# Performance work log

Measured on AMD Instinct MI355X. Metric: run time of the kernel, lower is better.

The kernel has to match this reference:

```python
import jax, jax.numpy as jnp
import numpy as np

B, T, C = 4, 2048, 768
N_HEAD = 12
HEAD_DIM = C // N_HEAD


def setup_inputs() -> dict:
    key = jax.random.key(0)
    k1, k2, k3 = jax.random.split(key, 3)
    x = jax.random.normal(k1, (B, T, C), dtype=jnp.float32)
    w_attn = jax.random.normal(k2, (C, 3 * C), dtype=jnp.float32) * (1.0 / np.sqrt(C))
    b_attn = jnp.zeros((3 * C,), dtype=jnp.float32)
    w_proj = jax.random.normal(k3, (C, C), dtype=jnp.float32) * (1.0 / np.sqrt(C))
    b_proj = jnp.zeros((C,), dtype=jnp.float32)
    return {"x": x, "w_attn": w_attn, "b_attn": b_attn, "w_proj": w_proj, "b_proj": b_proj}


def reference(x, w_attn, b_attn, w_proj, b_proj):
    # x: [B, T, C]
    Bs, Ts, Cs = x.shape
    qkv = x @ w_attn + b_attn                         # [B, T, 3C]
    q, k, v = jnp.split(qkv, 3, axis=-1)
    # -> [B, H, T, Dh]
    q = q.reshape(Bs, Ts, N_HEAD, HEAD_DIM).swapaxes(1, 2)
    k = k.reshape(Bs, Ts, N_HEAD, HEAD_DIM).swapaxes(1, 2)
    v = v.reshape(Bs, Ts, N_HEAD, HEAD_DIM).swapaxes(1, 2)
    scale = 1.0 / jnp.sqrt(jnp.asarray(HEAD_DIM, dtype=x.dtype))
    att = jnp.einsum('bhqd,bhkd->bhqk', q, k) * scale  # [B, H, T, T]
    causal = jnp.tril(jnp.ones((Ts, Ts), dtype=bool))[None, None]
    att = jnp.where(causal, att, jnp.asarray(-jnp.inf, dtype=att.dtype))
    att = jax.nn.softmax(att, axis=-1)
    y = jnp.einsum('bhqk,bhkd->bhqd', att, v)          # [B, H, T, Dh]
    y = y.swapaxes(1, 2).reshape(Bs, Ts, Cs)
    y = y @ w_proj + b_proj
    return y
```

## Files before the change

### kernel.cpp

```cpp
#include <hip/hip_runtime.h>
#include <cstdint>
#include <cstddef>

typedef __bf16 bf16x8 __attribute__((ext_vector_type(8)));
typedef float  f32x4  __attribute__((ext_vector_type(4)));
typedef unsigned short us;

#define DEV static __device__ __forceinline__

DEV us f2bf(float f) {
    unsigned int u = __builtin_bit_cast(unsigned int, f);
    u += 0x7FFFu + ((u >> 16) & 1u);
    return (us)(u >> 16);
}
DEV unsigned int pack2bf(float a, float b) {
    unsigned int ua = __builtin_bit_cast(unsigned int, a) + 0x8000u;
    unsigned int ub = __builtin_bit_cast(unsigned int, b) + 0x8000u;
    return (ua >> 16) | (ub & 0xFFFF0000u);
}

DEV void gll16(const void* g, void* l) {
    __builtin_amdgcn_global_load_lds(
        (const __attribute__((address_space(1))) unsigned int*)g,
        (__attribute__((address_space(3))) unsigned int*)l, 16, 0, 0);
}

DEV bf16x8 ld_frag(const us* p) {
    return __builtin_bit_cast(bf16x8, *reinterpret_cast<const uint4*>(p));
}

#define BB 4
#define TT 2048
#define CC 768
#define NH 12
#define DH 64
#define MM (BB*TT)
#define QSCALE 0.1803368801111144f

__global__ __launch_bounds__(256)
void cast_k(const float* __restrict__ x, us* __restrict__ xb, int n4)
{
    int i = blockIdx.x * 256 + threadIdx.x;
    int stride = gridDim.x * 256;
    for (; i < n4; i += stride) {
        float4 f = reinterpret_cast<const float4*>(x)[i];
        ushort4 o;
        o.x = f2bf(f.x); o.y = f2bf(f.y); o.z = f2bf(f.z); o.w = f2bf(f.w);
        reinterpret_cast<ushort4*>(xb)[i] = o;
    }
}

__global__ __launch_bounds__(256)
void transpose_k(const float* __restrict__ src,
                 us* __restrict__ dst, int R, int Cc)
{
    __shared__ float tile[32][33];
    int c0 = blockIdx.x * 32, r0 = blockIdx.y * 32;
    int tx = threadIdx.x, ty = threadIdx.y;
#pragma unroll
    for (int i = 0; i < 4; ++i)
        tile[ty + i*8][tx] = src[(size_t)(r0 + ty + i*8) * Cc + c0 + tx];
    __syncthreads();
#pragma unroll
    for (int i = 0; i < 4; ++i)
        dst[(size_t)(c0 + ty + i*8) * R + r0 + tx] = f2bf(tile[tx][ty + i*8]);
}


#define BM 128
#define BN 128
#define BK 32

template<int MODE>
__global__ __launch_bounds__(256)
void gemm_bt(const us* __restrict__ A,
             const us* __restrict__ Bt,
             const float* __restrict__ bias,
             float* __restrict__ Cout,
             us* __restrict__ Qo, us* __restrict__ Ko, us* __restrict__ Vo,
             int M, int N, int K)
{
    __shared__ __align__(16) us As[BM * BK];
    __shared__ __align__(16) us Bs[BN * BK];

    const int tid  = threadIdx.x;
    const int wave = tid >> 6, lane = tid & 63;
    const int quad = lane >> 4, l16 = lane & 15;
    const int waveM = (wave >> 1) * 64, waveN = (wave & 1) * 64;
    const int m0 = blockIdx.y * BM, n0 = blockIdx.x * BN;

    const f32x4 zero4 = {0.f, 0.f, 0.f, 0.f};
    f32x4 acc[4][4];
#pragma unroll
    for (int i = 0; i < 4; ++i)
#pragma unroll
        for (int j = 0; j < 4; ++j) acc[i][j] = zero4;

    const int lrow = lane >> 2, lch = (lane & 3) * 8;
    const int nk = K / BK;
    for (int kt = 0; kt < nk; ++kt) {
#pragma unroll
        for (int c = 0; c < 2; ++c) {
            int rb = (wave * 2 + c) * 16;
            int row = rb + lrow;
            gll16(A  + (size_t)(m0 + row) * K + kt * BK + lch, &As[rb * BK]);
            gll16(Bt + (size_t)(n0 + row) * K + kt * BK + lch, &Bs[rb * BK]);
        }
        __syncthreads();

        bf16x8 af[4], bfv[4];
#pragma unroll
        for (int mi = 0; mi < 4; ++mi)
            af[mi] = *reinterpret_cast<const bf16x8*>(&As[(waveM + mi * 16 + l16) * BK + quad * 8]);
#pragma unroll
        for (int ni = 0; ni < 4; ++ni)
            bfv[ni] = *reinterpret_cast<const bf16x8*>(&Bs[(waveN + ni * 16 + l16) * BK + quad * 8]);
#pragma unroll
        for (int mi = 0; mi < 4; ++mi)
#pragma unroll
            for (int ni = 0; ni < 4; ++ni)
                acc[mi][ni] = __builtin_amdgcn_mfma_f32_16x16x32_bf16(af[mi], bfv[ni], acc[mi][ni], 0, 0, 0);
        __syncthreads();
    }

#pragma unroll
    for (int mi = 0; mi < 4; ++mi) {
#pragma unroll
        for (int ni = 0; ni < 4; ++ni) {
            int n = n0 + waveN + ni * 16 + l16;
            float bv = bias[n];
            int mg = m0 + waveM + mi * 16 + quad * 4;
            if (MODE == 0) {
#pragma unroll
                for (int reg = 0; reg < 4; ++reg)
                    Cout[(size_t)(mg + reg) * N + n] = acc[mi][ni][reg] + bv;
            } else {
                int which = n / CC, c2 = n % CC;
                int h = c2 >> 6, d = c2 & 63;
                int b = mg >> 11, t0 = mg & 2047;
                size_t hb = (size_t)(b * NH + h) * TT * DH;
                if (which == 2) {
                    size_t off = hb + (size_t)(t0 >> 6) * 4096 + (d >> 4) * 1024
                               + ((t0 >> 3) & 7) * 128 + (d & 15) * 8 + (t0 & 7);
                    ushort4 pk;
                    pk.x = f2bf(acc[mi][ni][0] + bv);
                    pk.y = f2bf(acc[mi][ni][1] + bv);
                    pk.z = f2bf(acc[mi][ni][2] + bv);
                    pk.w = f2bf(acc[mi][ni][3] + bv);
                    *reinterpret_cast<ushort4*>(Vo + off) = pk;
                } else if (which == 1) {
                    size_t off = hb + (size_t)(t0 >> 4) * 1024 + (d >> 3) * 128
                               + (t0 & 15) * 8 + (d & 7);
#pragma unroll
                    for (int reg = 0; reg < 4; ++reg)
                        Ko[off + reg * 8] = f2bf(acc[mi][ni][reg] + bv);
                } else {
#pragma unroll
                    for (int reg = 0; reg < 4; ++reg) {
                        size_t off = hb + (size_t)(t0 + reg) * DH + d;
                        Qo[off] = f2bf((acc[mi][ni][reg] + bv) * QSCALE);
                    }
                }
            }
        }
    }
}

#define PST 72

__global__ __launch_bounds__(128)
void attn_k(const us* __restrict__ Qg,
            const us* __restrict__ Kg,
            const us* __restrict__ Vt,
            us* __restrict__ Og)
{
    __shared__ __align__(16) us Ps[2][32 * PST];

    const int tid  = threadIdx.x;
    const int wave = tid >> 6, lane = tid & 63;
    const int quad = lane >> 4, l16 = lane & 15;

    const int id  = blockIdx.x;
    const int xcd = id & 7, s = id >> 3;
    const int bh  = xcd + 8 * (s >> 4);
    const int q   = s & 15;
    const int pw  = 2 * q + wave;

    const size_t base = (size_t)bh * TT * DH;
    const int b = bh / NH, h = bh % NH;
    us* myP = Ps[wave];

    const f32x4 zero4 = {0.f, 0.f, 0.f, 0.f};

#pragma unroll 1
    for (int seg = 0; seg < 2; ++seg) {
        const int g   = seg ? 63 - pw : pw;
        const int nkt = (g >> 1) + 1;
        const int mA  = g * 32 + l16;
        const int mB  = mA + 16;

        bf16x8 qfA0 = ld_frag(Qg + base + (size_t)mA * DH + quad * 8);
        bf16x8 qfA1 = ld_frag(Qg + base + (size_t)mA * DH + 32 + quad * 8);
        bf16x8 qfB0 = ld_frag(Qg + base + (size_t)mB * DH + quad * 8);
        bf16x8 qfB1 = ld_frag(Qg + base + (size_t)mB * DH + 32 + quad * 8);

        f32x4 oA[4], oB[4];
#pragma unroll
        for (int i = 0; i < 4; ++i) { oA[i] = zero4; oB[i] = zero4; }
        float lrA = 0.f, lrB = 0.f;

#pragma unroll 1
        for (int j = 0; j < nkt; ++j) {
            const us* kb = Kg + base + (size_t)j * 4096;
            const us* vb = Vt + base + (size_t)j * 4096;

            bf16x8 kf[4][2];
#pragma unroll
            for (int sub = 0; sub < 4; ++sub)
#pragma unroll
                for (int hh = 0; hh < 2; ++hh)
                    kf[sub][hh] = ld_frag(kb + sub * 1024 + hh * 512 + lane * 8);

            f32x4 sA[4], sB[4];
#pragma unroll
            for (int sub = 0; sub < 4; ++sub) {
                f32x4 t = __builtin_amdgcn_mfma_f32_16x16x32_bf16(kf[sub][0], qfA0, zero4, 0, 0, 0);
                sA[sub]  = __builtin_amdgcn_mfma_f32_16x16x32_bf16(kf[sub][1], qfA1, t, 0, 0, 0);
                f32x4 u = __builtin_amdgcn_mfma_f32_16x16x32_bf16(kf[sub][0], qfB0, zero4, 0, 0, 0);
                sB[sub]  = __builtin_amdgcn_mfma_f32_16x16x32_bf16(kf[sub][1], qfB1, u, 0, 0, 0);
            }

            bf16x8 vf[4][2];
#pragma unroll
            for (int dsub = 0; dsub < 4; ++dsub)
#pragma unroll
                for (int kc = 0; kc < 2; ++kc)
                    vf[dsub][kc] = ld_frag(vb + dsub * 1024 + kc * 512 + lane * 8);

            if (j == nkt - 1) {
#pragma unroll
                for (int sub = 0; sub < 4; ++sub)
#pragma unroll
                    for (int reg = 0; reg < 4; ++reg) {
                        int key = j * 64 + sub * 16 + quad * 4 + reg;
                        if (key > mA) sA[sub][reg] = -INFINITY;
                        if (key > mB) sB[sub][reg] = -INFINITY;
                    }
            }

            {
                float rs = 0.f;
#pragma unroll
                for (int sub = 0; sub < 4; ++sub) {
                    float p0 = exp2f(sA[sub][0]), p1 = exp2f(sA[sub][1]);
                    float p2 = exp2f(sA[sub][2]), p3 = exp2f(sA[sub][3]);
                    rs += (p0 + p1) + (p2 + p3);
                    uint2 pk; pk.x = pack2bf(p0, p1); pk.y = pack2bf(p2, p3);
                    *reinterpret_cast<uint2*>(&myP[l16 * PST + sub * 16 + quad * 4]) = pk;
                }
                rs += __shfl_xor(rs, 16);
                rs += __shfl_xor(rs, 32);
                lrA += rs;
            }
            {
                float rs = 0.f;
#pragma unroll
                for (int sub = 0; sub < 4; ++sub) {
                    float p0 = exp2f(sB[sub][0]), p1 = exp2f(sB[sub][1]);
                    float p2 = exp2f(sB[sub][2]), p3 = exp2f(sB[sub][3]);
                    rs += (p0 + p1) + (p2 + p3);
                    uint2 pk; pk.x = pack2bf(p0, p1); pk.y = pack2bf(p2, p3);
                    *reinterpret_cast<uint2*>(&myP[(16 + l16) * PST + sub * 16 + quad * 4]) = pk;
                }
                rs += __shfl_xor(rs, 16);
                rs += __shfl_xor(rs, 32);
                lrB += rs;
            }

#pragma unroll
            for (int kc = 0; kc < 2; ++kc) {
                bf16x8 pfA = *reinterpret_cast<const bf16x8*>(&myP[l16 * PST + kc * 32 + quad * 8]);
                bf16x8 pfB = *reinterpret_cast<const bf16x8*>(&myP[(16 + l16) * PST + kc * 32 + quad * 8]);
#pragma unroll
                for (int d = 0; d < 4; ++d) {
                    oA[d] = __builtin_amdgcn_mfma_f32_16x16x32_bf16(vf[d][kc], pfA, oA[d], 0, 0, 0);
                    oB[d] = __builtin_amdgcn_mfma_f32_16x16x32_bf16(vf[d][kc], pfB, oB[d], 0, 0, 0);
                }
            }
        }

        const float invA = 1.f / lrA, invB = 1.f / lrB;
        us* orowA = Og + ((size_t)(b * TT + mA)) * CC + h * DH;
        us* orowB = Og + ((size_t)(b * TT + mB)) * CC + h * DH;
#pragma unroll
        for (int d = 0; d < 4; ++d) {
            uint2 pa, pb;
            pa.x = pack2bf(oA[d][0] * invA, oA[d][1] * invA);
            pa.y = pack2bf(oA[d][2] * invA, oA[d][3] * invA);
            pb.x = pack2bf(oB[d][0] * invB, oB[d][1] * invB);
            pb.y = pack2bf(oB[d][2] * invB, oB[d][3] * invB);
            *reinterpret_cast<uint2*>(orowA + d * 16 + quad * 4) = pa;
            *reinterpret_cast<uint2*>(orowB + d * 16 + quad * 4) = pb;
        }
    }
}

extern "C" void kernel_launch(void* const* d_in, const int* in_sizes, int n_in,
                              void* d_out, int out_size, void* d_ws, size_t ws_size,
                              hipStream_t stream)
{
    const float* x      = (const float*)d_in[0];
    const float* w_attn = (const float*)d_in[1];
    const float* b_attn = (const float*)d_in[2];
    const float* w_proj = (const float*)d_in[3];
    const float* b_proj = (const float*)d_in[4];
    float* out = (float*)d_out;

    char* ws = (char*)d_ws;
    size_t off = 0;
    auto alloc = [&](size_t bytes) {
        void* p = ws + off;
        off += (bytes + 255) & ~(size_t)255;
        return p;
    };
    us* wtA = (us*)alloc((size_t)(3 * CC) * CC * 2);
    us* wtP = (us*)alloc((size_t)CC * CC * 2);
    us* xb  = (us*)alloc((size_t)MM * CC * 2);
    us* Qb  = (us*)alloc((size_t)MM * CC * 2);
    us* Kb  = (us*)alloc((size_t)MM * CC * 2);
    us* Vtb = (us*)alloc((size_t)MM * CC * 2);
    us* att = (us*)alloc((size_t)MM * CC * 2);

    cast_k<<<1024, 256, 0, stream>>>(x, xb, MM * CC / 4);
    transpose_k<<<dim3((3 * CC) / 32, CC / 32), dim3(32, 8), 0, stream>>>(w_attn, wtA, CC, 3 * CC);
    transpose_k<<<dim3(CC / 32, CC / 32), dim3(32, 8), 0, stream>>>(w_proj, wtP, CC, CC);

    gemm_bt<1><<<dim3((3 * CC) / BN, MM / BM), 256, 0, stream>>>(
        xb, wtA, b_attn, nullptr, Qb, Kb, Vtb, MM, 3 * CC, CC);

    attn_k<<<dim3(16 * BB * NH), 128, 0, stream>>>(Qb, Kb, Vtb, att);

    gemm_bt<0><<<dim3(CC / BN, MM / BM), 256, 0, stream>>>(
        att, wtP, b_proj, out, nullptr, nullptr, nullptr, MM, CC, CC);

    (void)in_sizes; (void)n_in; (void)out_size; (void)ws_size;
}
```

Baseline: 232.1 us.

## Split long causal query rows across two waves with shared-memory merge

Each block now handles one high query tile and one low tile. Wave 0 covers the first 16 key tiles of the high tile. Wave 1 computes the whole low tile and then the remaining key tiles of the high tile, and the two partial sums and outputs are merged through shared memory. The grid is doubled so work is spread more evenly over more blocks. This is possible because the softmax uses no running max, so partial sums add directly. It costs extra LDS, a block barrier and the merge step.

```diff
diff --git a/kernel.cpp b/kernel.cpp
--- a/kernel.cpp
+++ b/kernel.cpp
@@ -168,6 +168,121 @@
 
 #define PST 72
 
+DEV void attn_tiles(const us* __restrict__ Qh, const us* __restrict__ Kh,
+                    const us* __restrict__ Vh, us* __restrict__ myP,
+                    int g, int j0, int j1, int maskLast,
+                    int quad, int l16, int lane,
+                    float& lrA, float& lrB, f32x4* oA, f32x4* oB)
+{
+    const f32x4 zero4 = {0.f, 0.f, 0.f, 0.f};
+    const int mA = g * 32 + l16;
+    const int mB = mA + 16;
+
+    bf16x8 qfA0 = ld_frag(Qh + (size_t)mA * DH + quad * 8);
+    bf16x8 qfA1 = ld_frag(Qh + (size_t)mA * DH + 32 + quad * 8);
+    bf16x8 qfB0 = ld_frag(Qh + (size_t)mB * DH + quad * 8);
+    bf16x8 qfB1 = ld_frag(Qh + (size_t)mB * DH + 32 + quad * 8);
+
+#pragma unroll 1
+    for (int j = j0; j < j1; ++j) {
+        const us* kb = Kh + (size_t)j * 4096;
+        const us* vb = Vh + (size_t)j * 4096;
+
+        bf16x8 kf[4][2];
+#pragma unroll
+        for (int sub = 0; sub < 4; ++sub)
+#pragma unroll
+            for (int hh = 0; hh < 2; ++hh)
+                kf[sub][hh] = ld_frag(kb + sub * 1024 + hh * 512 + lane * 8);
+
+        f32x4 sA[4], sB[4];
+#pragma unroll
+        for (int sub = 0; sub < 4; ++sub) {
+            f32x4 t = __builtin_amdgcn_mfma_f32_16x16x32_bf16(kf[sub][0], qfA0, zero4, 0, 0, 0);
+            sA[sub]  = __builtin_amdgcn_mfma_f32_16x16x32_bf16(kf[sub][1], qfA1, t, 0, 0, 0);
+            f32x4 u = __builtin_amdgcn_mfma_f32_16x16x32_bf16(kf[sub][0], qfB0, zero4, 0, 0, 0);
+            sB[sub]  = __builtin_amdgcn_mfma_f32_16x16x32_bf16(kf[sub][1], qfB1, u, 0, 0, 0);
+        }
+
+        bf16x8 vf[4][2];
+#pragma unroll
+        for (int dsub = 0; dsub < 4; ++dsub)
+#pragma unroll
+            for (int kc = 0; kc < 2; ++kc)
+                vf[dsub][kc] = ld_frag(vb + dsub * 1024 + kc * 512 + lane * 8);
+
+        if (maskLast && j == j1 - 1) {
+#pragma unroll
+            for (int sub = 0; sub < 4; ++sub)
+#pragma unroll
+                for (int reg = 0; reg < 4; ++reg) {
+                    int key = j * 64 + sub * 16 + quad * 4 + reg;
+                    if (key > mA) sA[sub][reg] = -INFINITY;
+                    if (key > mB) sB[sub][reg] = -INFINITY;
+                }
+        }
+
+        {
+            float rs = 0.f;
+#pragma unroll
+            for (int sub = 0; sub < 4; ++sub) {
+                float p0 = exp2f(sA[sub][0]), p1 = exp2f(sA[sub][1]);
+                float p2 = exp2f(sA[sub][2]), p3 = exp2f(sA[sub][3]);
+                rs += (p0 + p1) + (p2 + p3);
+                uint2 pk; pk.x = pack2bf(p0, p1); pk.y = pack2bf(p2, p3);
+                *reinterpret_cast<uint2*>(&myP[l16 * PST + sub * 16 + quad * 4]) = pk;
+            }
+            rs += __shfl_xor(rs, 16);
+            rs += __shfl_xor(rs, 32);
+            lrA += rs;
+        }
+        {
+            float rs = 0.f;
+#pragma unroll
+            for (int sub = 0; sub < 4; ++sub) {
+                float p0 = exp2f(sB[sub][0]), p1 = exp2f(sB[sub][1]);
+                float p2 = exp2f(sB[sub][2]), p3 = exp2f(sB[sub][3]);
+                rs += (p0 + p1) + (p2 + p3);
+                uint2 pk; pk.x = pack2bf(p0, p1); pk.y = pack2bf(p2, p3);
+                *reinterpret_cast<uint2*>(&myP[(16 + l16) * PST + sub * 16 + quad * 4]) = pk;
+            }
+            rs += __shfl_xor(rs, 16);
+            rs += __shfl_xor(rs, 32);
+            lrB += rs;
+        }
+
+#pragma unroll
+        for (int kc = 0; kc < 2; ++kc) {
+            bf16x8 pfA = *reinterpret_cast<const bf16x8*>(&myP[l16 * PST + kc * 32 + quad * 8]);
+            bf16x8 pfB = *reinterpret_cast<const bf16x8*>(&myP[(16 + l16) * PST + kc * 32 + quad * 8]);
+#pragma unroll
+            for (int d = 0; d < 4; ++d) {
+                oA[d] = __builtin_amdgcn_mfma_f32_16x16x32_bf16(vf[d][kc], pfA, oA[d], 0, 0, 0);
+                oB[d] = __builtin_amdgcn_mfma_f32_16x16x32_bf16(vf[d][kc], pfB, oB[d], 0, 0, 0);
+            }
+        }
+    }
+}
+
+DEV void attn_store(us* __restrict__ Og, int b, int h, int mA, int quad,
+                    float lrA, float lrB, const f32x4* oA, const f32x4* oB)
+{
+    const int mB = mA + 16;
+    const float invA = 1.f / lrA, invB = 1.f / lrB;
+    us* orowA = Og + ((size_t)(b * TT + mA)) * CC + h * DH;
+    us* orowB = Og + ((size_t)(b * TT + mB)) * CC + h * DH;
+#pragma unroll
+    for (int d = 0; d < 4; ++d) {
+        uint2 pa, pb;
+        pa.x = pack2bf(oA[d][0] * invA, oA[d][1] * invA);
+        pa.y = pack2bf(oA[d][2] * invA, oA[d][3] * invA);
+        pb.x = pack2bf(oB[d][0] * invB, oB[d][1] * invB);
+        pb.y = pack2bf(oB[d][2] * invB, oB[d][3] * invB);
+        *reinterpret_cast<uint2*>(orowA + d * 16 + quad * 4) = pa;
+        *reinterpret_cast<uint2*>(orowB + d * 16 + quad * 4) = pb;
+    }
+}
+
 __global__ __launch_bounds__(128)
 void attn_k(const us* __restrict__ Qg,
             const us* __restrict__ Kg,
@@ -175,6 +290,7 @@
             us* __restrict__ Og)
 {
     __shared__ __align__(16) us Ps[2][32 * PST];
+    __shared__ float Mrg[64 * 35];
 
     const int tid  = threadIdx.x;
     const int wave = tid >> 6, lane = tid & 63;
@@ -182,126 +298,64 @@
 
     const int id  = blockIdx.x;
     const int xcd = id & 7, s = id >> 3;
-    const int bh  = xcd + 8 * (s >> 4);
-    const int q   = s & 15;
-    const int pw  = 2 * q + wave;
-
-    const size_t base = (size_t)bh * TT * DH;
+    const int bh  = xcd + 8 * (s >> 5);
+    const int pw  = s & 31;
+
+    const int g_hi = 32 + pw;
+    const int g_lo = 63 - g_hi;
+    const int nkt_hi = (g_hi >> 1) + 1;
+    const int nkt_lo = (g_lo >> 1) + 1;
+
+    const us* Qh = Qg + (size_t)bh * TT * DH;
+    const us* Kh = Kg + (size_t)bh * TT * DH;
+    const us* Vh = Vt + (size_t)bh * TT * DH;
     const int b = bh / NH, h = bh % NH;
     us* myP = Ps[wave];
 
     const f32x4 zero4 = {0.f, 0.f, 0.f, 0.f};
-
-#pragma unroll 1
-    for (int seg = 0; seg < 2; ++seg) {
-        const int g   = seg ? 63 - pw : pw;
-        const int nkt = (g >> 1) + 1;
-        const int mA  = g * 32 + l16;
-        const int mB  = mA + 16;
-
-        bf16x8 qfA0 = ld_frag(Qg + base + (size_t)mA * DH + quad * 8);
-        bf16x8 qfA1 = ld_frag(Qg + base + (size_t)mA * DH + 32 + quad * 8);
-        bf16x8 qfB0 = ld_frag(Qg + base + (size_t)mB * DH + quad * 8);
-        bf16x8 qfB1 = ld_frag(Qg + base + (size_t)mB * DH + 32 + quad * 8);
-
-        f32x4 oA[4], oB[4];
+    f32x4 oA[4], oB[4];
+#pragma unroll
+    for (int i = 0; i < 4; ++i) { oA[i] = zero4; oB[i] = zero4; }
+    float lrA = 0.f, lrB = 0.f;
+
+    if (wave == 0) {
+        attn_tiles(Qh, Kh, Vh, myP, g_hi, 0, 16, 0, quad, l16, lane,
+                   lrA, lrB, oA, oB);
+    } else {
+        attn_tiles(Qh, Kh, Vh, myP, g_lo, 0, nkt_lo, 1, quad, l16, lane,
+                   lrA, lrB, oA, oB);
+        attn_store(Og, b, h, g_lo * 32 + l16, quad, lrA, lrB, oA, oB);
+
 #pragma unroll
         for (int i = 0; i < 4; ++i) { oA[i] = zero4; oB[i] = zero4; }
-        float lrA = 0.f, lrB = 0.f;
-
-#pragma unroll 1
-        for (int j = 0; j < nkt; ++j) {
-            const us* kb = Kg + base + (size_t)j * 4096;
-            const us* vb = Vt + base + (size_t)j * 4096;
-
-            bf16x8 kf[4][2];
-#pragma unroll
-            for (int sub = 0; sub < 4; ++sub)
-#pragma unroll
-                for (int hh = 0; hh < 2; ++hh)
-                    kf[sub][hh] = ld_frag(kb + sub * 1024 + hh * 512 + lane * 8);
-
-            f32x4 sA[4], sB[4];
-#pragma unroll
-            for (int sub = 0; sub < 4; ++sub) {
-                f32x4 t = __builtin_amdgcn_mfma_f32_16x16x32_bf16(kf[sub][0], qfA0, zero4, 0, 0, 0);
-                sA[sub]  = __builtin_amdgcn_mfma_f32_16x16x32_bf16(kf[sub][1], qfA1, t, 0, 0, 0);
-                f32x4 u = __builtin_amdgcn_mfma_f32_16x16x32_bf16(kf[sub][0], qfB0, zero4, 0, 0, 0);
-                sB[sub]  = __builtin_amdgcn_mfma_f32_16x16x32_bf16(kf[sub][1], qfB1, u, 0, 0, 0);
-            }
-
-            bf16x8 vf[4][2];
-#pragma unroll
-            for (int dsub = 0; dsub < 4; ++dsub)
-#pragma unroll
-                for (int kc = 0; kc < 2; ++kc)
-                    vf[dsub][kc] = ld_frag(vb + dsub * 1024 + kc * 512 + lane * 8);
-
-            if (j == nkt - 1) {
-#pragma unroll
-                for (int sub = 0; sub < 4; ++sub)
-#pragma unroll
-                    for (int reg = 0; reg < 4; ++reg) {
-                        int key = j * 64 + sub * 16 + quad * 4 + reg;
-                        if (key > mA) sA[sub][reg] = -INFINITY;
-                        if (key > mB) sB[sub][reg] = -INFINITY;
-                    }
-            }
-
-            {
-                float rs = 0.f;
-#pragma unroll
-                for (int sub = 0; sub < 4; ++sub) {
-                    float p0 = exp2f(sA[sub][0]), p1 = exp2f(sA[sub][1]);
-                    float p2 = exp2f(sA[sub][2]), p3 = exp2f(sA[sub][3]);
-                    rs += (p0 + p1) + (p2 + p3);
-                    uint2 pk; pk.x = pack2bf(p0, p1); pk.y = pack2bf(p2, p3);
-                    *reinterpret_cast<uint2*>(&myP[l16 * PST + sub * 16 + quad * 4]) = pk;
-                }
-                rs += __shfl_xor(rs, 16);
-                rs += __shfl_xor(rs, 32);
-                lrA += rs;
-            }
-            {
-                float rs = 0.f;
-#pragma unroll
-                for (int sub = 0; sub < 4; ++sub) {
-                    float p0 = exp2f(sB[sub][0]), p1 = exp2f(sB[sub][1]);
-                    float p2 = exp2f(sB[sub][2]), p3 = exp2f(sB[sub][3]);
-                    rs += (p0 + p1) + (p2 + p3);
-                    uint2 pk; pk.x = pack2bf(p0, p1); pk.y = pack2bf(p2, p3);
-                    *reinterpret_cast<uint2*>(&myP[(16 + l16) * PST + sub * 16 + quad * 4]) = pk;
-                }
-                rs += __shfl_xor(rs, 16);
-                rs += __shfl_xor(rs, 32);
-                lrB += rs;
-            }
-
-#pragma unroll
-            for (int kc = 0; kc < 2; ++kc) {
-                bf16x8 pfA = *reinterpret_cast<const bf16x8*>(&myP[l16 * PST + kc * 32 + quad * 8]);
-                bf16x8 pfB = *reinterpret_cast<const bf16x8*>(&myP[(16 + l16) * PST + kc * 32 + quad * 8]);
-#pragma unroll
-                for (int d = 0; d < 4; ++d) {
-                    oA[d] = __builtin_amdgcn_mfma_f32_16x16x32_bf16(vf[d][kc], pfA, oA[d], 0, 0, 0);
-                    oB[d] = __builtin_amdgcn_mfma_f32_16x16x32_bf16(vf[d][kc], pfB, oB[d], 0, 0, 0);
-                }
-            }
-        }
-
-        const float invA = 1.f / lrA, invB = 1.f / lrB;
-        us* orowA = Og + ((size_t)(b * TT + mA)) * CC + h * DH;
-        us* orowB = Og + ((size_t)(b * TT + mB)) * CC + h * DH;
-#pragma unroll
-        for (int d = 0; d < 4; ++d) {
-            uint2 pa, pb;
-            pa.x = pack2bf(oA[d][0] * invA, oA[d][1] * invA);
-            pa.y = pack2bf(oA[d][2] * invA, oA[d][3] * invA);
-            pb.x = pack2bf(oB[d][0] * invB, oB[d][1] * invB);
-            pb.y = pack2bf(oB[d][2] * invB, oB[d][3] * invB);
-            *reinterpret_cast<uint2*>(orowA + d * 16 + quad * 4) = pa;
-            *reinterpret_cast<uint2*>(orowB + d * 16 + quad * 4) = pb;
-        }
+        lrA = 0.f; lrB = 0.f;
+        attn_tiles(Qh, Kh, Vh, myP, g_hi, 16, nkt_hi, 1, quad, l16, lane,
+                   lrA, lrB, oA, oB);
+
+        float* mp = &Mrg[lane * 35];
+        mp[0] = lrA; mp[17] = lrB;
+#pragma unroll
+        for (int d = 0; d < 4; ++d)
+#pragma unroll
+            for (int r = 0; r < 4; ++r) {
+                mp[1 + d * 4 + r]  = oA[d][r];
+                mp[18 + d * 4 + r] = oB[d][r];
+            }
+    }
+
+    __syncthreads();
+
+    if (wave == 0) {
+        const float* mp = &Mrg[lane * 35];
+        lrA += mp[0]; lrB += mp[17];
+#pragma unroll
+        for (int d = 0; d < 4; ++d)
+#pragma unroll
+            for (int r = 0; r < 4; ++r) {
+                oA[d][r] += mp[1 + d * 4 + r];
+                oB[d][r] += mp[18 + d * 4 + r];
+            }
+        attn_store(Og, b, h, g_hi * 32 + l16, quad, lrA, lrB, oA, oB);
     }
 }
 
@@ -338,7 +392,7 @@
     gemm_bt<1><<<dim3((3 * CC) / BN, MM / BM), 256, 0, stream>>>(
         xb, wtA, b_attn, nullptr, Qb, Kb, Vtb, MM, 3 * CC, CC);
 
-    attn_k<<<dim3(16 * BB * NH), 128, 0, stream>>>(Qb, Kb, Vtb, att);
+    attn_k<<<dim3(32 * BB * NH), 128, 0, stream>>>(Qb, Kb, Vtb, att);
 
     gemm_bt<0><<<dim3(CC / BN, MM / BM), 256, 0, stream>>>(
         att, wtP, b_proj, out, nullptr, nullptr, nullptr, MM, CC, CC);
```

New measurement: 237.3 us. +2.3%, slower.

## Double-buffer K/V register fragments to prefetch next tile during compute

Applied to the files above, without the earlier changes.

Restructures the attention inner loop so K and V fragments for the next key tile are loaded into a second register set while the current tile's QK, softmax and PV run, ping-ponging between two buffers with a loop unrolled by two. This aims to hide global load latency behind MFMA and exp work. It doubles the register footprint of the K/V fragments, which may cut occupancy or cause spills, and on the last tile it issues a redundant prefetch of tile 0.

```diff
diff --git a/kernel.cpp b/kernel.cpp
--- a/kernel.cpp
+++ b/kernel.cpp
@@ -168,6 +168,91 @@
 
 #define PST 72
 
+DEV void tile_step(const us* __restrict__ Kh, const us* __restrict__ Vh,
+                   int jpref, int lane, int quad, int l16,
+                   bf16x8 (&kf)[4][2], bf16x8 (&vf)[4][2],
+                   bf16x8 (&kfN)[4][2], bf16x8 (&vfN)[4][2],
+                   const bf16x8& qfA0, const bf16x8& qfA1,
+                   const bf16x8& qfB0, const bf16x8& qfB1,
+                   int domask, int keybase, int mA, int mB,
+                   us* __restrict__ myP,
+                   float& lrA, float& lrB, f32x4* oA, f32x4* oB)
+{
+    const f32x4 zero4 = {0.f, 0.f, 0.f, 0.f};
+
+    {
+        const us* kbN = Kh + (size_t)jpref * 4096;
+        const us* vbN = Vh + (size_t)jpref * 4096;
+#pragma unroll
+        for (int sub = 0; sub < 4; ++sub) {
+            kfN[sub][0] = ld_frag(kbN + sub * 1024 +       lane * 8);
+            kfN[sub][1] = ld_frag(kbN + sub * 1024 + 512 + lane * 8);
+            vfN[sub][0] = ld_frag(vbN + sub * 1024 +       lane * 8);
+            vfN[sub][1] = ld_frag(vbN + sub * 1024 + 512 + lane * 8);
+        }
+    }
+
+    f32x4 sA[4], sB[4];
+#pragma unroll
+    for (int sub = 0; sub < 4; ++sub) {
+        f32x4 t = __builtin_amdgcn_mfma_f32_16x16x32_bf16(kf[sub][0], qfA0, zero4, 0, 0, 0);
+        sA[sub]  = __builtin_amdgcn_mfma_f32_16x16x32_bf16(kf[sub][1], qfA1, t, 0, 0, 0);
+        f32x4 u = __builtin_amdgcn_mfma_f32_16x16x32_bf16(kf[sub][0], qfB0, zero4, 0, 0, 0);
+        sB[sub]  = __builtin_amdgcn_mfma_f32_16x16x32_bf16(kf[sub][1], qfB1, u, 0, 0, 0);
+    }
+
+    if (domask) {
+#pragma unroll
+        for (int sub = 0; sub < 4; ++sub)
+#pragma unroll
+            for (int reg = 0; reg < 4; ++reg) {
+                int key = keybase + sub * 16 + quad * 4 + reg;
+                if (key > mA) sA[sub][reg] = -INFINITY;
+                if (key > mB) sB[sub][reg] = -INFINITY;
+            }
+    }
+
+    {
+        float rs = 0.f;
+#pragma unroll
+        for (int sub = 0; sub < 4; ++sub) {
+            float p0 = exp2f(sA[sub][0]), p1 = exp2f(sA[sub][1]);
+            float p2 = exp2f(sA[sub][2]), p3 = exp2f(sA[sub][3]);
+            rs += (p0 + p1) + (p2 + p3);
+            uint2 pk; pk.x = pack2bf(p0, p1); pk.y = pack2bf(p2, p3);
+            *reinterpret_cast<uint2*>(&myP[l16 * PST + sub * 16 + quad * 4]) = pk;
+        }
+        rs += __shfl_xor(rs, 16);
+        rs += __shfl_xor(rs, 32);
+        lrA += rs;
+    }
+    {
+        float rs = 0.f;
+#pragma unroll
+        for (int sub = 0; sub < 4; ++sub) {
+            float p0 = exp2f(sB[sub][0]), p1 = exp2f(sB[sub][1]);
+            float p2 = exp2f(sB[sub][2]), p3 = exp2f(sB[sub][3]);
+            rs += (p0 + p1) + (p2 + p3);
+            uint2 pk; pk.x = pack2bf(p0, p1); pk.y = pack2bf(p2, p3);
+            *reinterpret_cast<uint2*>(&myP[(16 + l16) * PST + sub * 16 + quad * 4]) = pk;
+        }
+        rs += __shfl_xor(rs, 16);
+        rs += __shfl_xor(rs, 32);
+        lrB += rs;
+    }
+
+#pragma unroll
+    for (int kc = 0; kc < 2; ++kc) {
+        bf16x8 pfA = *reinterpret_cast<const bf16x8*>(&myP[l16 * PST + kc * 32 + quad * 8]);
+        bf16x8 pfB = *reinterpret_cast<const bf16x8*>(&myP[(16 + l16) * PST + kc * 32 + quad * 8]);
+#pragma unroll
+        for (int d = 0; d < 4; ++d) {
+            oA[d] = __builtin_amdgcn_mfma_f32_16x16x32_bf16(vf[d][kc], pfA, oA[d], 0, 0, 0);
+            oB[d] = __builtin_amdgcn_mfma_f32_16x16x32_bf16(vf[d][kc], pfB, oB[d], 0, 0, 0);
+        }
+    }
+}
+
 __global__ __launch_bounds__(128)
 void attn_k(const us* __restrict__ Qg,
             const us* __restrict__ Kg,
@@ -186,7 +271,9 @@
     const int q   = s & 15;
     const int pw  = 2 * q + wave;
 
-    const size_t base = (size_t)bh * TT * DH;
+    const us* Qh = Qg + (size_t)bh * TT * DH;
+    const us* Kh = Kg + (size_t)bh * TT * DH;
+    const us* Vh = Vt + (size_t)bh * TT * DH;
     const int b = bh / NH, h = bh % NH;
     us* myP = Ps[wave];
 
@@ -199,94 +286,40 @@
         const int mA  = g * 32 + l16;
         const int mB  = mA + 16;
 
-        bf16x8 qfA0 = ld_frag(Qg + base + (size_t)mA * DH + quad * 8);
-        bf16x8 qfA1 = ld_frag(Qg + base + (size_t)mA * DH + 32 + quad * 8);
-        bf16x8 qfB0 = ld_frag(Qg + base + (size_t)mB * DH + quad * 8);
-        bf16x8 qfB1 = ld_frag(Qg + base + (size_t)mB * DH + 32 + quad * 8);
+        bf16x8 qfA0 = ld_frag(Qh + (size_t)mA * DH + quad * 8);
+        bf16x8 qfA1 = ld_frag(Qh + (size_t)mA * DH + 32 + quad * 8);
+        bf16x8 qfB0 = ld_frag(Qh + (size_t)mB * DH + quad * 8);
+        bf16x8 qfB1 = ld_frag(Qh + (size_t)mB * DH + 32 + quad * 8);
 
         f32x4 oA[4], oB[4];
 #pragma unroll
         for (int i = 0; i < 4; ++i) { oA[i] = zero4; oB[i] = zero4; }
         float lrA = 0.f, lrB = 0.f;
 
+        bf16x8 kf0[4][2], vf0[4][2], kf1[4][2], vf1[4][2];
+#pragma unroll
+        for (int sub = 0; sub < 4; ++sub) {
+            kf0[sub][0] = ld_frag(Kh + sub * 1024 +       lane * 8);
+            kf0[sub][1] = ld_frag(Kh + sub * 1024 + 512 + lane * 8);
+            vf0[sub][0] = ld_frag(Vh + sub * 1024 +       lane * 8);
+            vf0[sub][1] = ld_frag(Vh + sub * 1024 + 512 + lane * 8);
+        }
+
+        int j = 0;
 #pragma unroll 1
-        for (int j = 0; j < nkt; ++j) {
-            const us* kb = Kg + base + (size_t)j * 4096;
-            const us* vb = Vt + base + (size_t)j * 4096;
-
-            bf16x8 kf[4][2];
-#pragma unroll
-            for (int sub = 0; sub < 4; ++sub)
-#pragma unroll
-                for (int hh = 0; hh < 2; ++hh)
-                    kf[sub][hh] = ld_frag(kb + sub * 1024 + hh * 512 + lane * 8);
-
-            f32x4 sA[4], sB[4];
-#pragma unroll
-            for (int sub = 0; sub < 4; ++sub) {
-                f32x4 t = __builtin_amdgcn_mfma_f32_16x16x32_bf16(kf[sub][0], qfA0, zero4, 0, 0, 0);
-                sA[sub]  = __builtin_amdgcn_mfma_f32_16x16x32_bf16(kf[sub][1], qfA1, t, 0, 0, 0);
-                f32x4 u = __builtin_amdgcn_mfma_f32_16x16x32_bf16(kf[sub][0], qfB0, zero4, 0, 0, 0);
-                sB[sub]  = __builtin_amdgcn_mfma_f32_16x16x32_bf16(kf[sub][1], qfB1, u, 0, 0, 0);
-            }
-
-            bf16x8 vf[4][2];
-#pragma unroll
-            for (int dsub = 0; dsub < 4; ++dsub)
-#pragma unroll
-                for (int kc = 0; kc < 2; ++kc)
-                    vf[dsub][kc] = ld_frag(vb + dsub * 1024 + kc * 512 + lane * 8);
-
-            if (j == nkt - 1) {
-#pragma unroll
-                for (int sub = 0; sub < 4; ++sub)
-#pragma unroll
-                    for (int reg = 0; reg < 4; ++reg) {
-                        int key = j * 64 + sub * 16 + quad * 4 + reg;
-                        if (key > mA) sA[sub][reg] = -INFINITY;
-                        if (key > mB) sB[sub][reg] = -INFINITY;
-                    }
-            }
-
-            {
-                float rs = 0.f;
-#pragma unroll
-                for (int sub = 0; sub < 4; ++sub) {
-                    float p0 = exp2f(sA[sub][0]), p1 = exp2f(sA[sub][1]);
-                    float p2 = exp2f(sA[sub][2]), p3 = exp2f(sA[sub][3]);
-                    rs += (p0 + p1) + (p2 + p3);
-                    uint2 pk; pk.x = pack2bf(p0, p1); pk.y = pack2bf(p2, p3);
-                    *reinterpret_cast<uint2*>(&myP[l16 * PST + sub * 16 + quad * 4]) = pk;
-                }
-                rs += __shfl_xor(rs, 16);
-                rs += __shfl_xor(rs, 32);
-                lrA += rs;
-            }
-            {
-                float rs = 0.f;
-#pragma unroll
-                for (int sub = 0; sub < 4; ++sub) {
-                    float p0 = exp2f(sB[sub][0]), p1 = exp2f(sB[sub][1]);
-                    float p2 = exp2f(sB[sub][2]), p3 = exp2f(sB[sub][3]);
-                    rs += (p0 + p1) + (p2 + p3);
-                    uint2 pk; pk.x = pack2bf(p0, p1); pk.y = pack2bf(p2, p3);
-                    *reinterpret_cast<uint2*>(&myP[(16 + l16) * PST + sub * 16 + quad * 4]) = pk;
-                }
-                rs += __shfl_xor(rs, 16);
-                rs += __shfl_xor(rs, 32);
-                lrB += rs;
-            }
-
-#pragma unroll
-            for (int kc = 0; kc < 2; ++kc) {
-                bf16x8 pfA = *reinterpret_cast<const bf16x8*>(&myP[l16 * PST + kc * 32 + quad * 8]);
-                bf16x8 pfB = *reinterpret_cast<const bf16x8*>(&myP[(16 + l16) * PST + kc * 32 + quad * 8]);
-#pragma unroll
-                for (int d = 0; d < 4; ++d) {
-                    oA[d] = __builtin_amdgcn_mfma_f32_16x16x32_bf16(vf[d][kc], pfA, oA[d], 0, 0, 0);
-                    oB[d] = __builtin_amdgcn_mfma_f32_16x16x32_bf16(vf[d][kc], pfB, oB[d], 0, 0, 0);
-                }
-            }
+        for (; j + 2 <= nkt; j += 2) {
+            tile_step(Kh, Vh, j + 1, lane, quad, l16,
+                      kf0, vf0, kf1, vf1, qfA0, qfA1, qfB0, qfB1,
+                      0, j * 64, mA, mB, myP, lrA, lrB, oA, oB);
+            int jn = (j + 2 < nkt) ? (j + 2) : 0;
+            tile_step(Kh, Vh, jn, lane, quad, l16,
+                      kf1, vf1, kf0, vf0, qfA0, qfA1, qfB0, qfB1,
+                      (j + 2 == nkt) ? 1 : 0, (j + 1) * 64, mA, mB, myP, lrA, lrB, oA, oB);
+        }
+        if (j < nkt) {
+            tile_step(Kh, Vh, 0, lane, quad, l16,
+                      kf0, vf0, kf1, vf1, qfA0, qfA1, qfB0, qfB1,
+                      1, j * 64, mA, mB, myP, lrA, lrB, oA, oB);
         }
 
         const float invA = 1.f / lrA, invB = 1.f / lrB;
```

New measurement: 245.4 us. 5.8% more time.
